# Kernel optimization log

Measured on AMD Instinct MI355X. Metric: run time of the kernel, lower is better.

Reference implementation:

```python
import jax, jax.numpy as jnp
import numpy as np

N = 8192        # nodes
V = 50000       # vocab = len(dict_node_names)
EMB = 256       # embedding_dim
XI = EMB // 2   # x_increased_dim = 128
DIN = EMB + XI  # 384, SelfAtt_ dim
H = 4           # n_heads
D = 128         # WGAT output_dim per head (fusion dim)
E = 131072      # edges
CHUNK = 32768   # chunk_size (E % CHUNK == 0)


def _ln(x, g, b, eps=1e-5):
    m = jnp.mean(x, axis=-1, keepdims=True)
    v = jnp.mean((x - m) ** 2, axis=-1, keepdims=True)
    return (x - m) * jax.lax.rsqrt(v + eps) * g + b


def _wgat(emb, src, dst, edge_attr, wi, bi, wj, bj, wt, bt, attn):
    # x_i = features at destination (aggregation target), x_j = source/neighbor
    x_i = emb[dst]                                   # [E, din]
    x_j = emb[src]                                   # [E, din]
    h = (x_i @ wi + bi).reshape(E, H, D) + (x_j @ wj + bj).reshape(E, H, D)
    a = jnp.einsum('ehd,hd->eh', h, attn)            # [E, H]
    a = a * edge_attr[:, None]                       # edge weights pre-softmax
    # faithful chunked softmax: normalize over edges WITHIN each chunk (dim=0 per chunk)
    a = jax.nn.softmax(a.reshape(E // CHUNK, CHUNK, H), axis=1).reshape(E, H)
    xt = (x_j @ wt + bt).reshape(E, H, D)            # [E, H, D]
    msg = jnp.einsum('ehd,eh->ed', xt, a)            # sum over heads -> [E, D]
    return jax.ops.segment_sum(msg, dst, num_segments=N)  # aggr='add'


def _emb_forward(ids, edge_index, x, edge_attr, embed,
                 qkv_w, qkv_b, proj_w, proj_b, fuse_w, fuse_b, ln1_g, ln1_b,
                 wi0, bi0, wj0, bj0, wt0, bt0, attn0, skip0_w, skip0_b,
                 wi1, bi1, wj1, bj1, wt1, bt1, attn1, skip1_w, skip1_b,
                 ln2_g, ln2_b):
    E_i = embed[ids]                                 # [N, EMB] gather
    z = jnp.concatenate([jnp.tile(x, (1, XI)), E_i], axis=-1)   # [N, DIN]
    # SelfAtt_ : full N x N attention over nodes, scale = DIN**-0.5
    qkv = z @ qkv_w + qkv_b
    q, k, v = jnp.split(qkv, 3, axis=-1)
    att = jax.nn.softmax((q @ k.T) * (DIN ** -0.5), axis=-1) @ v
    z = att @ proj_w + proj_b                        # [N, DIN]
    emb = jax.nn.silu(_ln(z @ fuse_w + fuse_b, ln1_g, ln1_b)) + E_i  # [N, EMB]
    src, dst = edge_index[0], edge_index[1]
    emb = _wgat(emb, src, dst, edge_attr, wi0, bi0, wj0, bj0, wt0, bt0, attn0)  # [N, D]
    s0 = emb @ skip0_w + skip0_b
    emb = _wgat(emb, src, dst, edge_attr, wi1, bi1, wj1, bj1, wt1, bt1, attn1)  # [N, D]
    s1 = emb @ skip1_w + skip1_b
    emb = _ln(emb + (s0 + s1) * 0.5, ln2_g, ln2_b)
    return emb


def setup_inputs() -> dict:
    key = jax.random.key(0)
    ks = jax.random.split(key, 32)

    def w(k, shape, scale=0.05):
        return jax.random.normal(k, shape, jnp.float32) * scale

    inp = {}
    inp['ids'] = jax.random.randint(ks[0], (N,), 0, V)
    inp['x'] = jax.random.normal(ks[1], (N, 1), jnp.float32)
    inp['edge_attr'] = jax.random.uniform(ks[2], (E,), jnp.float32)
    inp['edge_index'] = jax.random.randint(ks[3], (2, E), 0, N)
    inp['embed'] = w(ks[4], (V, EMB), 1.0)
    inp['qkv_w'] = w(ks[5], (DIN, 3 * DIN)); inp['qkv_b'] = jnp.zeros((3 * DIN,), jnp.float32)
    inp['proj_w'] = w(ks[6], (DIN, DIN));    inp['proj_b'] = jnp.zeros((DIN,), jnp.float32)
    inp['fuse_w'] = w(ks[7], (DIN, EMB));    inp['fuse_b'] = jnp.zeros((EMB,), jnp.float32)
    inp['ln1_g'] = jnp.ones((EMB,), jnp.float32); inp['ln1_b'] = jnp.zeros((EMB,), jnp.float32)
    # WGAT layer 0: in=EMB, out=D per head, H heads
    inp['wi0'] = w(ks[8], (EMB, H * D));  inp['bi0'] = jnp.zeros((H * D,), jnp.float32)
    inp['wj0'] = w(ks[9], (EMB, H * D));  inp['bj0'] = jnp.zeros((H * D,), jnp.float32)
    inp['wt0'] = w(ks[10], (EMB, H * D)); inp['bt0'] = jnp.zeros((H * D,), jnp.float32)
    inp['attn0'] = w(ks[11], (H, D), 0.1)
    inp['skip0_w'] = w(ks[12], (D, D));   inp['skip0_b'] = jnp.zeros((D,), jnp.float32)
    # WGAT layer 1: in=D
    inp['wi1'] = w(ks[13], (D, H * D));   inp['bi1'] = jnp.zeros((H * D,), jnp.float32)
    inp['wj1'] = w(ks[14], (D, H * D));   inp['bj1'] = jnp.zeros((H * D,), jnp.float32)
    inp['wt1'] = w(ks[15], (D, H * D));   inp['bt1'] = jnp.zeros((H * D,), jnp.float32)
    inp['attn1'] = w(ks[16], (H, D), 0.1)
    inp['skip1_w'] = w(ks[17], (D, D));   inp['skip1_b'] = jnp.zeros((D,), jnp.float32)
    inp['ln2_g'] = jnp.ones((D,), jnp.float32); inp['ln2_b'] = jnp.zeros((D,), jnp.float32)
    return inp


def reference(ids, x, edge_attr, edge_index, embed,
              qkv_w, qkv_b, proj_w, proj_b, fuse_w, fuse_b, ln1_g, ln1_b,
              wi0, bi0, wj0, bj0, wt0, bt0, attn0, skip0_w, skip0_b,
              wi1, bi1, wj1, bj1, wt1, bt1, attn1, skip1_w, skip1_b,
              ln2_g, ln2_b):
    emb = _emb_forward(ids, edge_index, x, edge_attr, embed,
                       qkv_w, qkv_b, proj_w, proj_b, fuse_w, fuse_b, ln1_g, ln1_b,
                       wi0, bi0, wj0, bj0, wt0, bt0, attn0, skip0_w, skip0_b,
                       wi1, bi1, wj1, bj1, wt1, bt1, attn1, skip1_w, skip1_b,
                       ln2_g, ln2_b)
    return (emb, embed, ids)
```

## Files before the change

### kernel.cpp

```cpp
#include <hip/hip_runtime.h>

typedef __attribute__((ext_vector_type(8))) short bfrag;
typedef __attribute__((ext_vector_type(4))) float f4;

#define MFMA(a,b,c) __builtin_amdgcn_mfma_f32_16x16x32_bf16(a,b,c,0,0,0)

__device__ __forceinline__ unsigned short f2b(float x){
  union { float f; unsigned int u; } v; v.f = x;
  unsigned int r = v.u + 0x7fffu + ((v.u >> 16) & 1u);
  return (unsigned short)(r >> 16);
}
__device__ __forceinline__ float b2f(unsigned short h){
  union { unsigned int u; float f; } v; v.u = ((unsigned int)h) << 16;
  return v.f;
}

__global__ __launch_bounds__(256) void k_prep(
    const float* __restrict__ qkv_w, const float* __restrict__ proj_w,
    const float* __restrict__ proj_b, const float* __restrict__ fuse_w,
    const float* __restrict__ fuse_b,
    const float* __restrict__ wt0,
    const float* __restrict__ wt1, const float* __restrict__ sk0w,
    const float* __restrict__ wi0, const float* __restrict__ bi0,
    const float* __restrict__ wj0, const float* __restrict__ bj0,
    const float* __restrict__ wi1, const float* __restrict__ bi1,
    const float* __restrict__ wj1, const float* __restrict__ bj1,
    const float* __restrict__ attn0, const float* __restrict__ attn1,
    const float* __restrict__ bt0, const float* __restrict__ bt1,
    const float* __restrict__ sk0b,
    const float* __restrict__ embed, const int* __restrict__ ids,
    unsigned short* __restrict__ BtQKV, unsigned short* __restrict__ BtW2,
    unsigned short* __restrict__ BtT0, unsigned short* __restrict__ BtT1,
    float* __restrict__ biasW2,
    float* __restrict__ biasT0, float* __restrict__ biasT1,
    float* __restrict__ wsum, float* __restrict__ Ei)
{
  int b = blockIdx.x, t = threadIdx.x;
  if (b < 1152) {
    int idx = b*256 + t; int k = idx/1152, n = idx - k*1152;
    BtQKV[(size_t)n*256 + k] = f2b(qkv_w[128*1152 + idx]);
  } else if (b < 1536) {
    int k = b - 1152;
    float s = 0.f;
    for (int j = 0; j < 384; ++j) s += proj_w[(size_t)k*384 + j] * fuse_w[(size_t)j*256 + t];
    BtW2[(size_t)t*384 + k] = f2b(s);
  } else if (b == 1536) {
    float s = fuse_b[t];
    for (int j = 0; j < 384; ++j) s += proj_b[j] * fuse_w[(size_t)j*256 + t];
    biasW2[t] = s;
  } else if (b < 2049) {
    int idx = (b-1537)*256 + t; int k = idx/512, n = idx - k*512;
    BtT0[(size_t)n*256 + k] = f2b(wt0[idx]);
  } else if (b < 2305) {
    int idx = (b-2049)*256 + t; int k = idx/512, n = idx - k*512;
    BtT1[(size_t)n*128 + k] = f2b(wt1[idx]);
  } else if (b < 2369) {
    int idx = (b-2305)*256 + t; int k = idx/128, n = idx - k*128;
    BtT1[(size_t)(520+n)*128 + k] = f2b(sk0w[idx]);
  } else if (b < 2373) {
    int idx = (b-2369)*256 + t;
    int h = idx >> 8, k = idx & 255;
    float s = 0.f;
    for (int d = 0; d < 128; ++d) s += wi0[(size_t)k*512 + h*128 + d] * attn0[h*128 + d];
    BtT0[(size_t)(512 + h)*256 + k] = f2b(s);
    if (idx < 4) {
      float sb = 0.f;
      for (int d = 0; d < 128; ++d) sb += bi0[idx*128 + d] * attn0[idx*128 + d];
      biasT0[512 + idx] = sb;
    }
  } else if (b < 2377) {
    int idx = (b-2373)*256 + t;
    int h = idx >> 8, k = idx & 255;
    float s = 0.f;
    for (int d = 0; d < 128; ++d) s += wj0[(size_t)k*512 + h*128 + d] * attn0[h*128 + d];
    BtT0[(size_t)(516 + h)*256 + k] = f2b(s);
    if (idx < 4) {
      float sb = 0.f;
      for (int d = 0; d < 128; ++d) sb += bj0[idx*128 + d] * attn0[idx*128 + d];
      biasT0[516 + idx] = sb;
    }
  } else if (b < 2379) {
    int idx = (b-2377)*256 + t;
    int h = idx >> 7, k = idx & 127;
    float s = 0.f;
    for (int d = 0; d < 128; ++d) s += wi1[(size_t)k*512 + h*128 + d] * attn1[h*128 + d];
    BtT1[(size_t)(512 + h)*128 + k] = f2b(s);
    if (idx < 4) {
      float sb = 0.f;
      for (int d = 0; d < 128; ++d) sb += bi1[idx*128 + d] * attn1[idx*128 + d];
      biasT1[512 + idx] = sb;
    }
  } else if (b < 2381) {
    int idx = (b-2379)*256 + t;
    int h = idx >> 7, k = idx & 127;
    float s = 0.f;
    for (int d = 0; d < 128; ++d) s += wj1[(size_t)k*512 + h*128 + d] * attn1[h*128 + d];
    BtT1[(size_t)(516 + h)*128 + k] = f2b(s);
    if (idx < 4) {
      float sb = 0.f;
      for (int d = 0; d < 128; ++d) sb += bj1[idx*128 + d] * attn1[idx*128 + d];
      biasT1[516 + idx] = sb;
    }
  } else if (b < 2383) {
    int idx = (b-2381)*256 + t; biasT0[idx] = bt0[idx];
  } else if (b < 2385) {
    int idx = (b-2383)*256 + t; biasT1[idx] = bt1[idx];
  } else if (b == 2385) {
    if (t < 128) biasT1[520 + t] = sk0b[t];
  } else if (b < 2391) {
    int n = (b-2386)*256 + t;
    if (n < 1152) {
      float s = 0.f;
      for (int k = 0; k < 128; ++k) s += qkv_w[(size_t)k*1152 + n];
      wsum[n] = s;
    }
  } else {
    int idx = (b-2391)*256 + t;
    int n = idx >> 6, c4 = idx & 63;
    reinterpret_cast<float4*>(Ei)[idx] =
        reinterpret_cast<const float4*>(embed + (size_t)ids[n]*256)[c4];
  }
}

__global__ void k_outcopy(const float* __restrict__ embed, const int* __restrict__ ids,
                          float* __restrict__ out){
  int i = blockIdx.x*256 + threadIdx.x;
  if (i < 3200000)
    reinterpret_cast<float4*>(out)[262144 + i] = reinterpret_cast<const float4*>(embed)[i];
  if (i < 8192) out[13848576 + i] = (float)ids[i];
}

__global__ void k_deg(const int* __restrict__ ei, int* __restrict__ deg){
  int e = blockIdx.x*256 + threadIdx.x; if (e >= 131072) return;
  atomicAdd(&deg[ei[131072 + e]], 1);
}

__global__ __launch_bounds__(1024) void k_scan(const int* __restrict__ deg,
                                               int* __restrict__ off, int* __restrict__ cursor){
  int t = threadIdx.x;
  int v[8]; int s = 0;
  #pragma unroll
  for (int i=0;i<8;++i){ v[i] = s; s += deg[t*8 + i]; }
  int lane = t & 63, w = t >> 6;
  int si = s;
  for (int o=1;o<64;o<<=1){ int u = __shfl_up(si, o); if (lane >= o) si += u; }
  __shared__ int wsum[16];
  if (lane == 63) wsum[w] = si;
  __syncthreads();
  if (t < 16) {
    int x = wsum[t];
    for (int o=1;o<16;o<<=1){ int u = __shfl_up(x, o); if (t >= o) x += u; }
    wsum[t] = x;
  }
  __syncthreads();
  int wbase = (w == 0) ? 0 : wsum[w-1];
  int base = wbase + (si - s);
  #pragma unroll
  for (int i=0;i<8;++i){ int o2 = base + v[i]; off[t*8+i] = o2; cursor[t*8+i] = o2; }
  if (t == 1023) off[8192] = wbase + si;
}

__global__ void k_fill(const int* __restrict__ ei, int* __restrict__ cursor,
                       int* __restrict__ elist){
  int e = blockIdx.x*256 + threadIdx.x; if (e >= 131072) return;
  int d = ei[131072 + e];
  int slot = atomicAdd(&cursor[d], 1);
  elist[slot] = e;
}

__global__ __launch_bounds__(256) void k_gemm(
    const float* __restrict__ A, int lda,
    const unsigned short* __restrict__ Bt, int K,
    const float* __restrict__ bias,
    float* __restrict__ C, int ldc, int mode,
    const float* __restrict__ xv, const float* __restrict__ wsum,
    unsigned short* __restrict__ qO, unsigned short* __restrict__ kO,
    unsigned short* __restrict__ vO,
    const unsigned short* __restrict__ opA, const float* __restrict__ cw,
    float* __restrict__ aux, int ncols)
{
  __shared__ unsigned short As[128*40];
  __shared__ unsigned short Bs[128*40];
  const int t = threadIdx.x;
  const int wid = t >> 6, l = t & 63;
  const int lr = l & 15, lg = l >> 4;
  const int arow0 = blockIdx.y*128, bn0 = blockIdx.x*128;
  const int wr = (wid >> 1)*64, wc = (wid & 1)*64;
  f4 zero = {0.f,0.f,0.f,0.f};
  f4 acc[4][4];
  #pragma unroll
  for (int i=0;i<4;++i)
    #pragma unroll
    for (int j=0;j<4;++j) acc[i][j] = zero;

  for (int k0 = 0; k0 < K; k0 += 32) {
    #pragma unroll
    for (int p=0;p<4;++p) {
      int row = p*32 + (t>>3);
      int c4  = (t&7)*4;
      ushort4 h4;
      if (mode == 2) {
        const float* w4 = &cw[(arow0+row)*4];
        float a0=0.f,a1=0.f,a2=0.f,a3=0.f;
        #pragma unroll
        for (int s=0;s<4;++s) {
          ushort4 u = *reinterpret_cast<const ushort4*>(
              opA + (size_t)s*3145728 + (size_t)(arow0+row)*384 + k0 + c4);
          float wv = w4[s];
          a0 += b2f(u.x)*wv; a1 += b2f(u.y)*wv; a2 += b2f(u.z)*wv; a3 += b2f(u.w)*wv;
        }
        h4.x = f2b(a0); h4.y = f2b(a1); h4.z = f2b(a2); h4.w = f2b(a3);
      } else {
        float4 v = *reinterpret_cast<const float4*>(A + (size_t)(arow0+row)*lda + k0 + c4);
        h4.x = f2b(v.x); h4.y = f2b(v.y); h4.z = f2b(v.z); h4.w = f2b(v.w);
      }
      *reinterpret_cast<ushort4*>(&As[row*40 + c4]) = h4;
    }
    #pragma unroll
    for (int p=0;p<2;++p) {
      int n  = p*64 + (t>>2);
      int c8 = (t&3)*8;
      int4 v = *reinterpret_cast<const int4*>(Bt + (size_t)(bn0+n)*K + k0 + c8);
      *reinterpret_cast<int4*>(&Bs[n*40 + c8]) = v;
    }
    __syncthreads();
    bfrag af[4], bfm[4];
    #pragma unroll
    for (int mi=0;mi<4;++mi) af[mi] = *reinterpret_cast<const bfrag*>(&As[(wr+mi*16+lr)*40 + lg*8]);
    #pragma unroll
    for (int ni=0;ni<4;++ni) bfm[ni] = *reinterpret_cast<const bfrag*>(&Bs[(wc+ni*16+lr)*40 + lg*8]);
    #pragma unroll
    for (int mi=0;mi<4;++mi)
      #pragma unroll
      for (int ni=0;ni<4;++ni)
        acc[mi][ni] = MFMA(af[mi], bfm[ni], acc[mi][ni]);
    __syncthreads();
  }
  #pragma unroll
  for (int mi=0;mi<4;++mi) {
    #pragma unroll
    for (int ni=0;ni<4;++ni) {
      int col = bn0 + wc + ni*16 + lr;
      float bv = bias[col];
      float wsv = (mode==1) ? wsum[col] : 0.f;
      #pragma unroll
      for (int i=0;i<4;++i) {
        int row = arow0 + wr + mi*16 + lg*4 + i;
        float val = acc[mi][ni][i] + bv;
        if (mode == 1) {
          val += xv[row]*wsv;
          if (col < 384) val *= 0.05103103631f;
          unsigned short hv = f2b(val);
          if (col < 384)      qO[(size_t)row*384 + col] = hv;
          else if (col < 768) kO[(size_t)row*384 + col - 384] = hv;
          else {
            int d = col - 768, j = row;
            size_t vidx = (size_t)(j >> 5)*12288 + (size_t)(d >> 4)*512
                        + (size_t)(d & 15)*32 + (size_t)((j & 31) >> 3)*8 + (j & 7);
            vO[vidx] = hv;
          }
        } else if (mode == 3) {
          if (col < 512)      qO[(size_t)row*512 + col] = f2b(val);
          else if (col < 520) C[(size_t)row*8 + col - 512] = val;
          else if (col < ncols) aux[(size_t)row*128 + col - 520] = val;
        } else {
          C[(size_t)row*ldc + col] = val;
        }
      }
    }
  }
}

__global__ __launch_bounds__(256,2) void k_flash(
    const unsigned short* __restrict__ qg,
    const unsigned short* __restrict__ kg,
    const unsigned short* __restrict__ vg,
    unsigned short* __restrict__ Opart, float* __restrict__ mpart, float* __restrict__ lpart)
{
  __shared__ unsigned short Ks[32*384];
  __shared__ unsigned short Ps[64*40];
  __shared__ float f_s[64];

  const int t = threadIdx.x;
  const int w = t >> 6, l = t & 63;
  const int lr = l & 15, lg = l >> 4;
  const int qbi = blockIdx.x >> 2, split = blockIdx.x & 3;
  const int qbase = qbi * 64;

  #define STAGE_K(JJ) do { \
    _Pragma("unroll") \
    for (int p_=0;p_<6;++p_) { \
      int idx_ = p_*256 + t; \
      int row_ = idx_ / 48, uu_ = idx_ - row_*48; \
      int ug_ = uu_ ^ (row_ & 7); \
      const unsigned short* gp_ = kg + (size_t)((JJ) + row_)*384 + ug_*8; \
      __builtin_amdgcn_global_load_lds((const __attribute__((address_space(1))) void*)gp_, \
          (__attribute__((address_space(3))) void*)&Ks[idx_*8], 16, 0, 0); \
    } } while(0)

  bfrag qf[12];
  #pragma unroll
  for (int kk=0;kk<12;++kk)
    qf[kk] = *reinterpret_cast<const bfrag*>(qg + (size_t)(qbase + w*16 + lr)*384 + kk*32 + lg*8);

  f4 zero = {0.f,0.f,0.f,0.f};
  f4 o[4][6];
  #pragma unroll
  for (int a=0;a<4;++a)
    #pragma unroll
    for (int b=0;b<6;++b) o[a][b] = zero;

  float m = -3e38f, lsum = 0.f;
  const int j0beg = split*2048, jend = j0beg + 2048;

  STAGE_K(j0beg);
  __syncthreads();

  for (int j0 = j0beg; j0 < jend; j0 += 32) {
    f4 s0 = zero, s1 = zero;
    __builtin_amdgcn_s_setprio(1);
    #pragma unroll
    for (int kk=0;kk<12;++kk) {
      int su = ((kk*4 + lg) ^ (lr & 7)) * 8;
      bfrag k0 = *reinterpret_cast<const bfrag*>(&Ks[lr*384 + su]);
      bfrag k1 = *reinterpret_cast<const bfrag*>(&Ks[(16+lr)*384 + su]);
      s0 = MFMA(k0, qf[kk], s0);
      s1 = MFMA(k1, qf[kk], s1);
    }
    __builtin_amdgcn_s_setprio(0);

    float mt = fmaxf(fmaxf(fmaxf(s0[0],s0[1]),fmaxf(s0[2],s0[3])),
                     fmaxf(fmaxf(s1[0],s1[1]),fmaxf(s1[2],s1[3])));
    mt = fmaxf(mt, __shfl_xor(mt,16));
    mt = fmaxf(mt, __shfl_xor(mt,32));
    bool grew = mt > m + 8.f;
    bool doresc = __any(grew);
    float mn = doresc ? fmaxf(m, mt) : m;
    float p0[4], p1[4];
    float sum = 0.f;
    #pragma unroll
    for (int i=0;i<4;++i) {
      p0[i] = __expf(s0[i]-mn); p1[i] = __expf(s1[i]-mn);
      sum += p0[i] + p1[i];
    }
    sum += __shfl_xor(sum,16);
    sum += __shfl_xor(sum,32);
    float f = 1.f;
    if (doresc) {
      f = __expf(m - mn);
      lsum = lsum * f + sum;
      m = mn;
    } else {
      lsum += sum;
    }

    unsigned int pk0 = (unsigned int)f2b(p0[0]) | ((unsigned int)f2b(p0[1]) << 16);
    unsigned int pk1 = (unsigned int)f2b(p0[2]) | ((unsigned int)f2b(p0[3]) << 16);
    unsigned int pk2 = (unsigned int)f2b(p1[0]) | ((unsigned int)f2b(p1[1]) << 16);
    unsigned int pk3 = (unsigned int)f2b(p1[2]) | ((unsigned int)f2b(p1[3]) << 16);
    int prow = (w*16 + lr)*40;
    *reinterpret_cast<unsigned int*>(&Ps[prow + lg*4])          = pk0;
    *reinterpret_cast<unsigned int*>(&Ps[prow + lg*4 + 2])      = pk1;
    *reinterpret_cast<unsigned int*>(&Ps[prow + 16 + lg*4])     = pk2;
    *reinterpret_cast<unsigned int*>(&Ps[prow + 16 + lg*4 + 2]) = pk3;
    if (lg == 0) f_s[w*16 + lr] = f;

    __syncthreads();

    if (j0 + 32 < jend) STAGE_K(j0 + 32);

    const int jt = j0 >> 5;
    bfrag vf[6];
    #pragma unroll
    for (int dt=0;dt<6;++dt)
      vf[dt] = *reinterpret_cast<const bfrag*>(
          vg + (size_t)jt*12288 + (size_t)(w*6 + dt)*512 + lr*32 + lg*8);

    bfrag pf[4];
    #pragma unroll
    for (int qt=0;qt<4;++qt)
      pf[qt] = *reinterpret_cast<const bfrag*>(&Ps[(qt*16+lr)*40 + lg*8]);
    #pragma unroll
    for (int qt=0;qt<4;++qt) {
      #pragma unroll
      for (int i=0;i<4;++i) {
        float frv = f_s[qt*16 + lg*4 + i];
        #pragma unroll
        for (int dt=0;dt<6;++dt) o[qt][dt][i] *= frv;
      }
    }
    __builtin_amdgcn_s_setprio(1);
    #pragma unroll
    for (int qt=0;qt<4;++qt)
      #pragma unroll
      for (int dt=0;dt<6;++dt)
        o[qt][dt] = MFMA(pf[qt], vf[dt], o[qt][dt]);
    __builtin_amdgcn_s_setprio(0);

    __syncthreads();
  }
  #undef STAGE_K

  unsigned short* Op = Opart + (size_t)split*8192*384;
  #pragma unroll
  for (int qt=0;qt<4;++qt)
    #pragma unroll
    for (int dt=0;dt<6;++dt)
      #pragma unroll
      for (int i=0;i<4;++i)
        Op[(size_t)(qbase + qt*16 + lg*4 + i)*384 + w*96 + dt*16 + lr] = f2b(o[qt][dt][i]);
  if (lg == 0) {
    mpart[split*8192 + qbase + w*16 + lr] = m;
    lpart[split*8192 + qbase + w*16 + lr] = lsum;
  }
}

__global__ void k_cw(const float* __restrict__ mp, const float* __restrict__ lp,
                     float* __restrict__ cw)
{
  int r = blockIdx.x*256 + threadIdx.x;
  float m0 = mp[r], m1 = mp[8192+r], m2 = mp[16384+r], m3 = mp[24576+r];
  float M = fmaxf(fmaxf(m0,m1), fmaxf(m2,m3));
  float w0 = __expf(m0-M), w1 = __expf(m1-M), w2 = __expf(m2-M), w3 = __expf(m3-M);
  float L = lp[r]*w0 + lp[8192+r]*w1 + lp[16384+r]*w2 + lp[24576+r]*w3;
  float inv = 1.f / L;
  float4 o4 = make_float4(w0*inv, w1*inv, w2*inv, w3*inv);
  *reinterpret_cast<float4*>(&cw[r*4]) = o4;
}

__global__ __launch_bounds__(256) void k_ln1(const float* __restrict__ pre, const float* __restrict__ Ei,
                      const float* __restrict__ g, const float* __restrict__ b,
                      float* __restrict__ out)
{
  int row = blockIdx.x, c = threadIdx.x;
  float v = pre[(size_t)row*256 + c];
  float s1 = v, s2 = v*v;
  #pragma unroll
  for (int o1=32;o1;o1>>=1){ s1 += __shfl_down(s1,o1); s2 += __shfl_down(s2,o1); }
  __shared__ float a1[4], a2[4];
  if ((c&63)==0){ a1[c>>6] = s1; a2[c>>6] = s2; }
  __syncthreads();
  float S1 = a1[0]+a1[1]+a1[2]+a1[3], S2 = a2[0]+a2[1]+a2[2]+a2[3];
  float mean = S1*(1.f/256.f), var = S2*(1.f/256.f) - mean*mean;
  float y = (v-mean)*rsqrtf(var+1e-5f)*g[c] + b[c];
  float sig = 1.f/(1.f+__expf(-y));
  out[(size_t)row*256 + c] = y*sig + Ei[(size_t)row*256 + c];
}

__global__ void k_escore(const int* __restrict__ ei, const float* __restrict__ ea,
                         const float* __restrict__ SC, float* __restrict__ sc)
{
  int e = blockIdx.x*256 + threadIdx.x; if (e >= 131072) return;
  int s = ei[e], d = ei[131072 + e];
  float wv = ea[e];
  float4 ai = *reinterpret_cast<const float4*>(&SC[(size_t)d*8]);
  float4 aj = *reinterpret_cast<const float4*>(&SC[(size_t)s*8 + 4]);
  float4 o4 = make_float4((ai.x+aj.x)*wv, (ai.y+aj.y)*wv, (ai.z+aj.z)*wv, (ai.w+aj.w)*wv);
  *reinterpret_cast<float4*>(&sc[e*4]) = o4;
}

__global__ __launch_bounds__(1024) void k_cstats(const float* __restrict__ sc,
                        float* __restrict__ mx, float* __restrict__ sm)
{
  int ch = blockIdx.x;
  int c = ch >> 2, h = ch & 3;
  int t = threadIdx.x;
  const float* base = sc + (size_t)c*131072 + h;
  float lm = -3e38f, ls = 0.f;
  for (int i=t; i<32768; i+=1024) {
    float v = base[(size_t)i*4];
    if (v > lm) { ls = ls*__expf(lm - v) + 1.f; lm = v; }
    else        ls += __expf(v - lm);
  }
  #pragma unroll
  for (int o1=32;o1;o1>>=1) {
    float om = __shfl_down(lm,o1), os = __shfl_down(ls,o1);
    float M2 = fmaxf(lm, om);
    ls = ls*__expf(lm-M2) + os*__expf(om-M2);
    lm = M2;
  }
  __shared__ float rm[16], rs[16];
  if ((t&63)==0){ rm[t>>6] = lm; rs[t>>6] = ls; }
  __syncthreads();
  if (t == 0) {
    float M = rm[0], S = rs[0];
    for (int i=1;i<16;++i) {
      float M2 = fmaxf(M, rm[i]);
      S = S*__expf(M-M2) + rs[i]*__expf(rm[i]-M2);
      M = M2;
    }
    mx[ch] = M; sm[ch] = S;
  }
}

__global__ void k_pnorm(float* __restrict__ sc, const float* __restrict__ mx,
                        const float* __restrict__ sm)
{
  int i = blockIdx.x*256 + threadIdx.x;
  int e = i >> 2, h = i & 3;
  int ch = (e >> 15)*4 + h;
  sc[i] = __expf(sc[i] - mx[ch]) / sm[ch];
}

__global__ __launch_bounds__(128) void k_aggr(const int* __restrict__ off,
                      const int* __restrict__ elist, const int* __restrict__ ei,
                      const float* __restrict__ sc,
                      const unsigned short* __restrict__ Tb, float* __restrict__ g)
{
  int n = blockIdx.x, d = threadIdx.x;
  int qb = off[n], qe = off[n+1];
  float acc = 0.f;
  for (int q = qb; q < qe; ++q) {
    int e = elist[q];
    int s = ei[e];
    float4 p = *reinterpret_cast<const float4*>(&sc[e*4]);
    const unsigned short* Tr = Tb + (size_t)s*512;
    acc += p.x*b2f(Tr[d]) + p.y*b2f(Tr[128+d]) + p.z*b2f(Tr[256+d]) + p.w*b2f(Tr[384+d]);
  }
  g[(size_t)n*128 + d] = acc;
}

__global__ __launch_bounds__(128) void k_final(const float* __restrict__ g1, const float* __restrict__ aux,
                       const float* __restrict__ sw, const float* __restrict__ sb,
                       const float* __restrict__ lg2, const float* __restrict__ lb2,
                       float* __restrict__ out)
{
  int row = blockIdx.x, c = threadIdx.x;
  __shared__ float gr[128];
  float gv = g1[(size_t)row*128 + c];
  gr[c] = gv; __syncthreads();
  float s1 = sb[c];
  #pragma unroll 8
  for (int k=0;k<128;++k) s1 += gr[k]*sw[k*128 + c];
  float s0 = aux[(size_t)row*128 + c];
  float v = gv + 0.5f*(s0 + s1);
  float m1 = v, m2 = v*v;
  #pragma unroll
  for (int o1=32;o1;o1>>=1){ m1 += __shfl_down(m1,o1); m2 += __shfl_down(m2,o1); }
  __shared__ float a1[2], a2[2];
  if ((c&63)==0){ a1[c>>6]=m1; a2[c>>6]=m2; }
  __syncthreads();
  float S1 = a1[0]+a1[1], S2 = a2[0]+a2[1];
  float mean = S1*(1.f/128.f), var = S2*(1.f/128.f) - mean*mean;
  out[(size_t)row*128 + c] = (v-mean)*rsqrtf(var+1e-5f)*lg2[c] + lb2[c];
}

extern "C" void kernel_launch(void* const* d_in, const int* in_sizes, int n_in,
                              void* d_out, int out_size, void* d_ws, size_t ws_size,
                              hipStream_t stream)
{
  const int*   ids    = (const int*)  d_in[0];
  const float* x      = (const float*)d_in[1];
  const float* ea     = (const float*)d_in[2];
  const int*   eidx   = (const int*)  d_in[3];
  const float* embed  = (const float*)d_in[4];
  const float* qkv_w  = (const float*)d_in[5];
  const float* qkv_b  = (const float*)d_in[6];
  const float* proj_w = (const float*)d_in[7];
  const float* proj_b = (const float*)d_in[8];
  const float* fuse_w = (const float*)d_in[9];
  const float* fuse_b = (const float*)d_in[10];
  const float* ln1_g  = (const float*)d_in[11];
  const float* ln1_b  = (const float*)d_in[12];
  const float* wi0 = (const float*)d_in[13]; const float* bi0 = (const float*)d_in[14];
  const float* wj0 = (const float*)d_in[15]; const float* bj0 = (const float*)d_in[16];
  const float* wt0 = (const float*)d_in[17]; const float* bt0 = (const float*)d_in[18];
  const float* attn0 = (const float*)d_in[19];
  const float* sk0w = (const float*)d_in[20]; const float* sk0b = (const float*)d_in[21];
  const float* wi1 = (const float*)d_in[22]; const float* bi1 = (const float*)d_in[23];
  const float* wj1 = (const float*)d_in[24]; const float* bj1 = (const float*)d_in[25];
  const float* wt1 = (const float*)d_in[26]; const float* bt1 = (const float*)d_in[27];
  const float* attn1 = (const float*)d_in[28];
  const float* sk1w = (const float*)d_in[29]; const float* sk1b = (const float*)d_in[30];
  const float* ln2_g = (const float*)d_in[31]; const float* ln2_b = (const float*)d_in[32];

  char* ws = (char*)d_ws;
  const size_t MBy = (size_t)1 << 20;

  unsigned short* BtQKV  = (unsigned short*)(ws + 0);
  unsigned short* BtW2   = (unsigned short*)(ws + 589824);
  float* biasW2 = (float*)(ws + 884736);
  unsigned short* BtT0   = (unsigned short*)(ws + 1081344);
  unsigned short* BtT1   = (unsigned short*)(ws + 1409024);
  float* biasT0 = (float*)(ws + 1605632);
  float* biasT1 = (float*)(ws + 1608192);
  float* wsum   = (float*)(ws + 1611264);
  float* mxb    = (float*)(ws + 1615872);
  float* smb    = (float*)(ws + 1615936);
  int* deg    = (int*)(ws + 1703936);
  int* cursor = (int*)(ws + 1736704);
  int* off    = (int*)(ws + 1769472);
  float* cw   = (float*)(ws + 1806336);

  float* Ei   = (float*)(ws + 2*MBy);
  unsigned short* qb = (unsigned short*)(ws + 10*MBy);
  unsigned short* kb = (unsigned short*)(ws + 17*MBy);
  unsigned short* vb = (unsigned short*)(ws + 24*MBy);
  float* pre  = (float*)(ws + 31*MBy);
  float* emb0 = (float*)(ws + 39*MBy);
  unsigned short* TCb0 = (unsigned short*)(ws + 47*MBy);
  float* SCb0 = (float*)(ws + 55*MBy);
  float* SCb1 = (float*)(ws + 55*MBy + 262144);
  float* AUX  = (float*)(ws + 56*MBy);
  float* sc0  = (float*)(ws + 60*MBy);
  unsigned short* TCb1 = (unsigned short*)(ws + 10*MBy);
  float* sc1  = (float*)(ws + 24*MBy);
  float* g0   = (float*)(ws + 2*MBy);
  float* g1   = (float*)(ws + 6*MBy);
  int* elist  = (int*)(ws + 62*MBy);

  float* out = (float*)d_out;
  unsigned short* Opart = (unsigned short*)d_out;
  float* mpart = out + 6815744;
  float* lpart = out + 6848512;

  hipMemsetAsync(ws, 0, 2*MBy, stream);

  k_prep<<<4439, 256, 0, stream>>>(qkv_w, proj_w, proj_b, fuse_w, fuse_b,
                                   wt0, wt1, sk0w,
                                   wi0, bi0, wj0, bj0, wi1, bi1, wj1, bj1,
                                   attn0, attn1, bt0, bt1, sk0b, embed, ids,
                                   BtQKV, BtW2, BtT0, BtT1,
                                   biasW2, biasT0, biasT1, wsum, Ei);
  k_deg<<<512, 256, 0, stream>>>(eidx, deg);
  k_scan<<<1, 1024, 0, stream>>>(deg, off, cursor);
  k_fill<<<512, 256, 0, stream>>>(eidx, cursor, elist);

  k_gemm<<<dim3(9,64), 256, 0, stream>>>(Ei, 256, BtQKV, 256, qkv_b, nullptr, 0, 1,
                                         x, wsum, qb, kb, vb, nullptr, nullptr,
                                         nullptr, 0);
  k_flash<<<512, 256, 0, stream>>>(qb, kb, vb, Opart, mpart, lpart);
  k_cw<<<32, 256, 0, stream>>>(mpart, lpart, cw);

  k_gemm<<<dim3(2,64), 256, 0, stream>>>(nullptr, 0, BtW2, 384, biasW2, pre, 256, 2,
                                         nullptr, nullptr, nullptr, nullptr, nullptr,
                                         Opart, cw, nullptr, 0);
  k_outcopy<<<12500, 256, 0, stream>>>(embed, ids, out);
  k_ln1<<<8192, 256, 0, stream>>>(pre, Ei, ln1_g, ln1_b, emb0);

  k_gemm<<<dim3(5,64), 256, 0, stream>>>(emb0, 256, BtT0, 256, biasT0, SCb0, 0, 3,
                                         nullptr, nullptr, TCb0, nullptr, nullptr,
                                         nullptr, nullptr, AUX, 520);
  k_escore<<<512, 256, 0, stream>>>(eidx, ea, SCb0, sc0);
  k_cstats<<<16, 1024, 0, stream>>>(sc0, mxb, smb);
  k_pnorm<<<2048, 256, 0, stream>>>(sc0, mxb, smb);
  k_aggr<<<8192, 128, 0, stream>>>(off, elist, eidx, sc0, TCb0, g0);

  k_gemm<<<dim3(6,64), 256, 0, stream>>>(g0, 128, BtT1, 128, biasT1, SCb1, 0, 3,
                                         nullptr, nullptr, TCb1, nullptr, nullptr,
                                         nullptr, nullptr, AUX, 648);
  k_escore<<<512, 256, 0, stream>>>(eidx, ea, SCb1, sc1);
  k_cstats<<<16, 1024, 0, stream>>>(sc1, mxb, smb);
  k_pnorm<<<2048, 256, 0, stream>>>(sc1, mxb, smb);
  k_aggr<<<8192, 128, 0, stream>>>(off, elist, eidx, sc1, TCb1, g1);

  k_final<<<8192, 128, 0, stream>>>(g1, AUX, sk1w, sk1b, ln2_g, ln2_b, out);
}
```

Baseline: 458.6 us.

## Fuse softmax partial stats into edge scoring and merge output copy into prep

The edge-score kernel now also computes per-block online-softmax max/sum partials, so a small finalize kernel replaces the strided full re-read of the score array in the stats kernel. The embedding table copy to the output is folded into the prep kernel as extra blocks, removing one launch and letting it overlap with weight preprocessing. Flash-attention partials move from the output buffer into workspace, so the copy can happen early, and workspace buffers are rearranged to fit. This adds a shared-memory reduction and a barrier to the scoring kernel, and makes the prep grid much larger.

```diff
diff --git a/kernel.cpp b/kernel.cpp
--- a/kernel.cpp
+++ b/kernel.cpp
@@ -33,7 +33,8 @@
     unsigned short* __restrict__ BtT0, unsigned short* __restrict__ BtT1,
     float* __restrict__ biasW2,
     float* __restrict__ biasT0, float* __restrict__ biasT1,
-    float* __restrict__ wsum, float* __restrict__ Ei)
+    float* __restrict__ wsum, float* __restrict__ Ei,
+    float* __restrict__ out)
 {
   int b = blockIdx.x, t = threadIdx.x;
   if (b < 1152) {
@@ -114,20 +115,17 @@
       for (int k = 0; k < 128; ++k) s += qkv_w[(size_t)k*1152 + n];
       wsum[n] = s;
     }
-  } else {
+  } else if (b < 4439) {
     int idx = (b-2391)*256 + t;
     int n = idx >> 6, c4 = idx & 63;
     reinterpret_cast<float4*>(Ei)[idx] =
         reinterpret_cast<const float4*>(embed + (size_t)ids[n]*256)[c4];
-  }
-}
-
-__global__ void k_outcopy(const float* __restrict__ embed, const int* __restrict__ ids,
-                          float* __restrict__ out){
-  int i = blockIdx.x*256 + threadIdx.x;
-  if (i < 3200000)
-    reinterpret_cast<float4*>(out)[262144 + i] = reinterpret_cast<const float4*>(embed)[i];
-  if (i < 8192) out[13848576 + i] = (float)ids[i];
+  } else {
+    int i = (b-4439)*256 + t;
+    if (i < 3200000)
+      reinterpret_cast<float4*>(out)[262144 + i] = reinterpret_cast<const float4*>(embed)[i];
+    if (i < 8192) out[13848576 + i] = (float)ids[i];
+  }
 }
 
 __global__ void k_deg(const int* __restrict__ ei, int* __restrict__ deg){
@@ -447,49 +445,69 @@
   out[(size_t)row*256 + c] = y*sig + Ei[(size_t)row*256 + c];
 }
 
-__global__ void k_escore(const int* __restrict__ ei, const float* __restrict__ ea,
-                         const float* __restrict__ SC, float* __restrict__ sc)
-{
-  int e = blockIdx.x*256 + threadIdx.x; if (e >= 131072) return;
+__global__ __launch_bounds__(256) void k_escore(const int* __restrict__ ei, const float* __restrict__ ea,
+                         const float* __restrict__ SC, float* __restrict__ sc,
+                         float* __restrict__ pm, float* __restrict__ ps)
+{
+  int e = blockIdx.x*256 + threadIdx.x;
   int s = ei[e], d = ei[131072 + e];
   float wv = ea[e];
   float4 ai = *reinterpret_cast<const float4*>(&SC[(size_t)d*8]);
   float4 aj = *reinterpret_cast<const float4*>(&SC[(size_t)s*8 + 4]);
   float4 o4 = make_float4((ai.x+aj.x)*wv, (ai.y+aj.y)*wv, (ai.z+aj.z)*wv, (ai.w+aj.w)*wv);
   *reinterpret_cast<float4*>(&sc[e*4]) = o4;
-}
-
-__global__ __launch_bounds__(1024) void k_cstats(const float* __restrict__ sc,
-                        float* __restrict__ mx, float* __restrict__ sm)
+
+  float sv[4] = {o4.x, o4.y, o4.z, o4.w};
+  __shared__ float sm_[4][4], ss_[4][4];
+  int lane = threadIdx.x & 63, wvid = threadIdx.x >> 6;
+  #pragma unroll
+  for (int h=0; h<4; ++h) {
+    float m = sv[h], s2 = 1.f;
+    #pragma unroll
+    for (int o1=32;o1;o1>>=1) {
+      float om = __shfl_xor(m,o1), os = __shfl_xor(s2,o1);
+      float M2 = fmaxf(m,om);
+      s2 = s2*__expf(m-M2) + os*__expf(om-M2);
+      m = M2;
+    }
+    if (lane==0){ sm_[wvid][h]=m; ss_[wvid][h]=s2; }
+  }
+  __syncthreads();
+  if (threadIdx.x < 4) {
+    int h = threadIdx.x;
+    float M = sm_[0][h], S = ss_[0][h];
+    #pragma unroll
+    for (int i=1;i<4;++i){
+      float M2 = fmaxf(M, sm_[i][h]);
+      S = S*__expf(M-M2) + ss_[i][h]*__expf(sm_[i][h]-M2);
+      M = M2;
+    }
+    pm[blockIdx.x*4+h] = M; ps[blockIdx.x*4+h] = S;
+  }
+}
+
+__global__ __launch_bounds__(128) void k_cfin(const float* __restrict__ pm, const float* __restrict__ ps,
+                                              float* __restrict__ mx, float* __restrict__ sm)
 {
   int ch = blockIdx.x;
   int c = ch >> 2, h = ch & 3;
   int t = threadIdx.x;
-  const float* base = sc + (size_t)c*131072 + h;
-  float lm = -3e38f, ls = 0.f;
-  for (int i=t; i<32768; i+=1024) {
-    float v = base[(size_t)i*4];
-    if (v > lm) { ls = ls*__expf(lm - v) + 1.f; lm = v; }
-    else        ls += __expf(v - lm);
-  }
-  #pragma unroll
-  for (int o1=32;o1;o1>>=1) {
-    float om = __shfl_down(lm,o1), os = __shfl_down(ls,o1);
-    float M2 = fmaxf(lm, om);
-    ls = ls*__expf(lm-M2) + os*__expf(om-M2);
-    lm = M2;
-  }
-  __shared__ float rm[16], rs[16];
-  if ((t&63)==0){ rm[t>>6] = lm; rs[t>>6] = ls; }
+  float M = pm[(c*128 + t)*4 + h], S = ps[(c*128 + t)*4 + h];
+  int lane = t & 63;
+  #pragma unroll
+  for (int o1=32;o1;o1>>=1){
+    float om = __shfl_xor(M,o1), os = __shfl_xor(S,o1);
+    float M2 = fmaxf(M,om);
+    S = S*__expf(M-M2) + os*__expf(om-M2);
+    M = M2;
+  }
+  __shared__ float am[2], as[2];
+  if (lane==0){ am[t>>6]=M; as[t>>6]=S; }
   __syncthreads();
-  if (t == 0) {
-    float M = rm[0], S = rs[0];
-    for (int i=1;i<16;++i) {
-      float M2 = fmaxf(M, rm[i]);
-      S = S*__expf(M-M2) + rs[i]*__expf(rm[i]-M2);
-      M = M2;
-    }
-    mx[ch] = M; sm[ch] = S;
+  if (t==0){
+    float M2 = fmaxf(am[0],am[1]);
+    float Sf = as[0]*__expf(am[0]-M2) + as[1]*__expf(am[1]-M2);
+    mx[ch]=M2; sm[ch]=Sf;
   }
 }
 
@@ -591,37 +609,39 @@
   int* cursor = (int*)(ws + 1736704);
   int* off    = (int*)(ws + 1769472);
   float* cw   = (float*)(ws + 1806336);
+  float* pm   = (float*)(ws + 1937408);
+  float* ps   = (float*)(ws + 1945600);
 
   float* Ei   = (float*)(ws + 2*MBy);
   unsigned short* qb = (unsigned short*)(ws + 10*MBy);
   unsigned short* kb = (unsigned short*)(ws + 17*MBy);
   unsigned short* vb = (unsigned short*)(ws + 24*MBy);
-  float* pre  = (float*)(ws + 31*MBy);
-  float* emb0 = (float*)(ws + 39*MBy);
-  unsigned short* TCb0 = (unsigned short*)(ws + 47*MBy);
-  float* SCb0 = (float*)(ws + 55*MBy);
-  float* SCb1 = (float*)(ws + 55*MBy + 262144);
-  float* AUX  = (float*)(ws + 56*MBy);
-  float* sc0  = (float*)(ws + 60*MBy);
-  unsigned short* TCb1 = (unsigned short*)(ws + 10*MBy);
-  float* sc1  = (float*)(ws + 24*MBy);
+  unsigned short* Opart = (unsigned short*)(ws + 31*MBy);
+  float* mpart = (float*)(ws + 55*MBy);
+  float* lpart = (float*)(ws + 55*MBy + 131072);
+  float* pre  = (float*)(ws + 10*MBy);
+  float* emb0 = (float*)(ws + 31*MBy);
+  unsigned short* TCb0 = (unsigned short*)(ws + 39*MBy);
+  float* SCb0 = (float*)(ws + 47*MBy);
+  float* SCb1 = (float*)(ws + 47*MBy + 262144);
+  float* AUX  = (float*)(ws + 47*MBy + 524288);
+  float* sc0  = (float*)(ws + 52*MBy);
+  float* sc1  = (float*)(ws + 54*MBy);
+  unsigned short* TCb1 = (unsigned short*)(ws + 18*MBy);
   float* g0   = (float*)(ws + 2*MBy);
   float* g1   = (float*)(ws + 6*MBy);
   int* elist  = (int*)(ws + 62*MBy);
 
   float* out = (float*)d_out;
-  unsigned short* Opart = (unsigned short*)d_out;
-  float* mpart = out + 6815744;
-  float* lpart = out + 6848512;
 
   hipMemsetAsync(ws, 0, 2*MBy, stream);
 
-  k_prep<<<4439, 256, 0, stream>>>(qkv_w, proj_w, proj_b, fuse_w, fuse_b,
-                                   wt0, wt1, sk0w,
-                                   wi0, bi0, wj0, bj0, wi1, bi1, wj1, bj1,
-                                   attn0, attn1, bt0, bt1, sk0b, embed, ids,
-                                   BtQKV, BtW2, BtT0, BtT1,
-                                   biasW2, biasT0, biasT1, wsum, Ei);
+  k_prep<<<16939, 256, 0, stream>>>(qkv_w, proj_w, proj_b, fuse_w, fuse_b,
+                                    wt0, wt1, sk0w,
+                                    wi0, bi0, wj0, bj0, wi1, bi1, wj1, bj1,
+                                    attn0, attn1, bt0, bt1, sk0b, embed, ids,
+                                    BtQKV, BtW2, BtT0, BtT1,
+                                    biasW2, biasT0, biasT1, wsum, Ei, out);
   k_deg<<<512, 256, 0, stream>>>(eidx, deg);
   k_scan<<<1, 1024, 0, stream>>>(deg, off, cursor);
   k_fill<<<512, 256, 0, stream>>>(eidx, cursor, elist);
@@ -635,22 +655,21 @@
   k_gemm<<<dim3(2,64), 256, 0, stream>>>(nullptr, 0, BtW2, 384, biasW2, pre, 256, 2,
                                          nullptr, nullptr, nullptr, nullptr, nullptr,
                                          Opart, cw, nullptr, 0);
-  k_outcopy<<<12500, 256, 0, stream>>>(embed, ids, out);
   k_ln1<<<8192, 256, 0, stream>>>(pre, Ei, ln1_g, ln1_b, emb0);
 
   k_gemm<<<dim3(5,64), 256, 0, stream>>>(emb0, 256, BtT0, 256, biasT0, SCb0, 0, 3,
                                          nullptr, nullptr, TCb0, nullptr, nullptr,
                                          nullptr, nullptr, AUX, 520);
-  k_escore<<<512, 256, 0, stream>>>(eidx, ea, SCb0, sc0);
-  k_cstats<<<16, 1024, 0, stream>>>(sc0, mxb, smb);
+  k_escore<<<512, 256, 0, stream>>>(eidx, ea, SCb0, sc0, pm, ps);
+  k_cfin<<<16, 128, 0, stream>>>(pm, ps, mxb, smb);
   k_pnorm<<<2048, 256, 0, stream>>>(sc0, mxb, smb);
   k_aggr<<<8192, 128, 0, stream>>>(off, elist, eidx, sc0, TCb0, g0);
 
   k_gemm<<<dim3(6,64), 256, 0, stream>>>(g0, 128, BtT1, 128, biasT1, SCb1, 0, 3,
                                          nullptr, nullptr, TCb1, nullptr, nullptr,
                                          nullptr, nullptr, AUX, 648);
-  k_escore<<<512, 256, 0, stream>>>(eidx, ea, SCb1, sc1);
-  k_cstats<<<16, 1024, 0, stream>>>(sc1, mxb, smb);
+  k_escore<<<512, 256, 0, stream>>>(eidx, ea, SCb1, sc1, pm, ps);
+  k_cfin<<<16, 128, 0, stream>>>(pm, ps, mxb, smb);
   k_pnorm<<<2048, 256, 0, stream>>>(sc1, mxb, smb);
   k_aggr<<<8192, 128, 0, stream>>>(off, elist, eidx, sc1, TCb1, g1);
 
```

New measurement: 425.1 us. 7.3% less time.
